# Optimization experiments

Measured on AMD Instinct MI355X. Metric: run time of the kernel, lower is better.

The kernel has to match this reference:

```python
import jax, jax.numpy as jnp
import numpy as np

B, H, S, DK, DV = 2, 16, 2048, 64, 64

def setup_inputs() -> dict:
    key = jax.random.key(0)
    kq, kk, kv, km = jax.random.split(key, 4)
    q = jax.random.normal(kq, (B, H, S, DK), dtype=jnp.float32)
    k = jax.random.normal(kk, (B, H, S, DK), dtype=jnp.float32)
    v = jax.random.normal(kv, (B, H, S, DV), dtype=jnp.float32)
    mask = jax.random.randint(km, (B, H, S, S), 0, 2).astype(jnp.bool_)
    return {"q": q, "k": k, "v": v, "mask": mask}

def reference(q, k, v, mask):
    d_k = q.shape[-1]
    # scores: [B, H, Sq, Sk]
    scores = jnp.einsum('bhqd,bhkd->bhqk', q, k) / np.sqrt(d_k).astype(jnp.float32)
    scores = jnp.where(mask, jnp.float32(-1e9), scores)
    attn = jax.nn.softmax(scores, axis=-1)
    return jnp.einsum('bhqk,bhkd->bhqd', attn, v)
```

## Files before the change

kernel.cpp:

```cpp
#include <hip/hip_runtime.h>


#define LOG2E 1.4426950408889634f
#define QSCALE (0.125f * LOG2E)

typedef __attribute__((ext_vector_type(8))) short short8;
typedef __attribute__((ext_vector_type(4))) short short4v;
typedef __attribute__((ext_vector_type(4))) float f32x4;

constexpr int S = 2048, D = 64;

__device__ __forceinline__ short bf16rne(float x) {
  union { float f; unsigned u; } cv; cv.f = x;
  unsigned u = cv.u;
  u += 0x7fffu + ((u >> 16) & 1u);
  return (short)(u >> 16);
}

__device__ __forceinline__ void glds16(const void* g, void* l) {
  __builtin_amdgcn_global_load_lds(
      (const __attribute__((address_space(1))) void*)g,
      (__attribute__((address_space(3))) void*)l, 16, 0, 0);
}

__global__ void detect_mask_fmt(const unsigned* __restrict__ m, int* __restrict__ flag) {
  unsigned v = m[threadIdx.x];
  unsigned long long big = __ballot(v > 1u && v != 0x3F800000u);
  unsigned long long isf = __ballot(v == 0x3F800000u);
  if (threadIdx.x == 0) *flag = (big != 0ull && isf == 0ull) ? 1 : 0;
}

__global__ void prep_k(const float* __restrict__ kp, short* __restrict__ kb) {
  size_t i = ((size_t)blockIdx.x * 256 + threadIdx.x) * 8;
  float4 a = *(const float4*)(kp + i);
  float4 b = *(const float4*)(kp + i + 4);
  short8 s;
  s[0] = bf16rne(a.x); s[1] = bf16rne(a.y); s[2] = bf16rne(a.z); s[3] = bf16rne(a.w);
  s[4] = bf16rne(b.x); s[5] = bf16rne(b.y); s[6] = bf16rne(b.z); s[7] = bf16rne(b.w);
  *(short8*)&kb[i] = s;
}

__global__ void prep_vt(const float* __restrict__ vp, short* __restrict__ vt) {
  __shared__ float tile[64][65];
  const int tid = threadIdx.x;
  const int bh = blockIdx.x >> 5, k0 = (blockIdx.x & 31) * 64;
  const float* src = vp + ((size_t)(bh * S + k0)) * D;
#pragma unroll
  for (int i = 0; i < 4; ++i) {
    int row = i * 16 + (tid >> 4);
    int col = (tid & 15) * 4;
    float4 x = *(const float4*)(src + row * D + col);
    tile[row][col] = x.x; tile[row][col + 1] = x.y;
    tile[row][col + 2] = x.z; tile[row][col + 3] = x.w;
  }
  __syncthreads();
#pragma unroll
  for (int i = 0; i < 4; ++i) {
    int dim = i * 16 + (tid >> 4);
    int kb4 = (tid & 15) * 4;
    short4v s;
#pragma unroll
    for (int j = 0; j < 4; ++j) s[j] = bf16rne(tile[kb4 + j][dim]);
    *(short4v*)&vt[((size_t)(bh * D + dim)) * S + k0 + kb4] = s;
  }
}

__launch_bounds__(256, 4)
__global__ void attn_fwd(const float* __restrict__ qp, const short* __restrict__ kb,
                         const short* __restrict__ vt, const void* __restrict__ mp,
                         float* __restrict__ op, const int* __restrict__ fmtp) {
  const int fmt  = *fmtp;
  const int tid  = threadIdx.x;
  const int lane = tid & 63;
  const int w    = tid >> 6;
  const int c    = lane & 15;
  const int quad = lane >> 4;

  const int bh = blockIdx.x >> 5;
  const int q0 = (blockIdx.x & 31) * 64;

  __shared__ short ks[64 * 64];
  __shared__ short vs[64 * 64];
  __shared__ short pst[4][16 * 72];

  const float* qg = qp + ((size_t)(bh * S + q0 + w * 16 + c)) * D;
  short8 qB[2];
#pragma unroll
  for (int kk = 0; kk < 2; ++kk) {
    const float* p = qg + kk * 32 + quad * 8;
    float4 x = *(const float4*)(p);
    float4 y = *(const float4*)(p + 4);
    short8 f;
    f[0] = bf16rne(x.x * QSCALE); f[1] = bf16rne(x.y * QSCALE);
    f[2] = bf16rne(x.z * QSCALE); f[3] = bf16rne(x.w * QSCALE);
    f[4] = bf16rne(y.x * QSCALE); f[5] = bf16rne(y.y * QSCALE);
    f[6] = bf16rne(y.z * QSCALE); f[7] = bf16rne(y.w * QSCALE);
    qB[kk] = f;
  }

  f32x4 O[4];
#pragma unroll
  for (int t = 0; t < 4; ++t) O[t] = (f32x4){0.f, 0.f, 0.f, 0.f};
  float L = 0.f;

  const int rsub = lane >> 3;
  const int csw  = (lane & 7) ^ rsub;
  const short* kbase = kb + ((size_t)(bh * S)) * D;
  const short* vbase = vt + ((size_t)(bh * D)) * S;

  const int sw0 = ((quad     ) ^ (c & 7)) * 8;
  const int sw1 = ((quad | 4 ) ^ (c & 7)) * 8;

  const size_t mrow = ((size_t)(bh * S + q0 + w * 16 + c)) * S;

  for (int it = 0; it < 32; ++it) {
    const int k0 = it * 64;
    __syncthreads();

#pragma unroll
    for (int h = 0; h < 2; ++h) {
      const int rbase = (h * 4 + w) * 8;
      const int row = rbase + rsub;
      glds16(kbase + (size_t)(k0 + row) * 64 + csw * 8,
             (char*)ks + (h * 4 + w) * 1024);
      glds16(vbase + (size_t)row * S + k0 + csw * 8,
             (char*)vs + (h * 4 + w) * 1024);
    }

    unsigned mb[4];
    if (fmt == 1) {
      const unsigned char* mq = (const unsigned char*)mp + mrow + k0 + 4 * quad;
#pragma unroll
      for (int t = 0; t < 4; ++t) mb[t] = *(const unsigned*)(mq + 16 * t);
    } else {
      const unsigned* mq = (const unsigned*)mp + mrow + k0 + 4 * quad;
#pragma unroll
      for (int t = 0; t < 4; ++t) {
        uint4 v = *(const uint4*)(mq + 16 * t);
        mb[t] = (v.x ? 1u : 0u) | (v.y ? 0x100u : 0u) |
                (v.z ? 0x10000u : 0u) | (v.w ? 0x1000000u : 0u);
      }
    }
    __syncthreads();

    float part = 0.f;
#pragma unroll
    for (int t = 0; t < 4; ++t) {
      short8 ka0 = *(const short8*)&ks[(16 * t + c) * 64 + sw0];
      short8 ka1 = *(const short8*)&ks[(16 * t + c) * 64 + sw1];
      f32x4 z = (f32x4){0.f, 0.f, 0.f, 0.f};
      z = __builtin_amdgcn_mfma_f32_16x16x32_bf16(ka0, qB[0], z, 0, 0, 0);
      z = __builtin_amdgcn_mfma_f32_16x16x32_bf16(ka1, qB[1], z, 0, 0, 0);
      short4v s4;
#pragma unroll
      for (int r = 0; r < 4; ++r) {
        float e = ((mb[t] >> (8 * r)) & 0xffu) ? 0.f : exp2f(z[r]);
        part += e;
        s4[r] = bf16rne(e);
      }
      *(short4v*)&pst[w][c * 72 + 16 * t + 4 * quad] = s4;
    }

    part += __shfl_xor(part, 16);
    part += __shfl_xor(part, 32);
    L += part;

    short8 pa0 = *(const short8*)&pst[w][c * 72 + quad * 8];
    short8 pa1 = *(const short8*)&pst[w][c * 72 + 32 + quad * 8];
#pragma unroll
    for (int t = 0; t < 4; ++t) {
      short8 vb0 = *(const short8*)&vs[(16 * t + c) * 64 + sw0];
      short8 vb1 = *(const short8*)&vs[(16 * t + c) * 64 + sw1];
      O[t] = __builtin_amdgcn_mfma_f32_16x16x32_bf16(pa0, vb0, O[t], 0, 0, 0);
      O[t] = __builtin_amdgcn_mfma_f32_16x16x32_bf16(pa1, vb1, O[t], 0, 0, 0);
    }
  }

#pragma unroll
  for (int r = 0; r < 4; ++r) {
    float Lr = __shfl(L, (lane & 48) | (quad * 4 + r));
    float inv = 1.f / Lr;
    const size_t ob = ((size_t)(bh * S + q0 + w * 16 + quad * 4 + r)) * D;
#pragma unroll
    for (int t = 0; t < 4; ++t) op[ob + 16 * t + c] = O[t][r] * inv;
  }
}

extern "C" void kernel_launch(void* const* d_in, const int* in_sizes, int n_in,
                              void* d_out, int out_size, void* d_ws, size_t ws_size,
                              hipStream_t stream) {
  const float* q = (const float*)d_in[0];
  const float* k = (const float*)d_in[1];
  const float* v = (const float*)d_in[2];
  const void*  m = d_in[3];

  short* kb  = (short*)d_ws;
  short* vtb = (short*)((char*)d_ws + (8u << 20));
  int* flag  = (int*)((char*)d_ws + (16u << 20));

  detect_mask_fmt<<<1, 64, 0, stream>>>((const unsigned*)m, flag);
  prep_k<<<2048, 256, 0, stream>>>(k, kb);
  prep_vt<<<1024, 256, 0, stream>>>(v, vtb);
  attn_fwd<<<1024, 256, 0, stream>>>(q, kb, vtb, m, (float*)d_out, flag);
}
```

Before: 754.7 us.

## Process 128 query rows per block and merge prep kernels into one launch

Each attention block now handles two 64-row query halves, so every K/V tile loaded into LDS feeds twice as many MFMAs. This halves the global-to-LDS K/V traffic per query and halves the grid to 512 blocks, with launch bounds lowered to 2 waves per SIMD for the extra registers. The three preprocessing kernels (mask format detection, K conversion, V transpose) are merged into one launch to cut launch overhead. The risks are lower occupancy, fewer blocks than CUs allow for latency hiding, and higher register pressure. The mask read, which dominates traffic, is unchanged.

Result: no change. 757.8 us (+0.4%).

```diff
diff --git a/kernel.cpp b/kernel.cpp
--- a/kernel.cpp
+++ b/kernel.cpp
@@ -23,49 +23,52 @@
       (__attribute__((address_space(3))) void*)l, 16, 0, 0);
 }
 
-__global__ void detect_mask_fmt(const unsigned* __restrict__ m, int* __restrict__ flag) {
-  unsigned v = m[threadIdx.x];
-  unsigned long long big = __ballot(v > 1u && v != 0x3F800000u);
-  unsigned long long isf = __ballot(v == 0x3F800000u);
-  if (threadIdx.x == 0) *flag = (big != 0ull && isf == 0ull) ? 1 : 0;
-}
-
-__global__ void prep_k(const float* __restrict__ kp, short* __restrict__ kb) {
-  size_t i = ((size_t)blockIdx.x * 256 + threadIdx.x) * 8;
-  float4 a = *(const float4*)(kp + i);
-  float4 b = *(const float4*)(kp + i + 4);
-  short8 s;
-  s[0] = bf16rne(a.x); s[1] = bf16rne(a.y); s[2] = bf16rne(a.z); s[3] = bf16rne(a.w);
-  s[4] = bf16rne(b.x); s[5] = bf16rne(b.y); s[6] = bf16rne(b.z); s[7] = bf16rne(b.w);
-  *(short8*)&kb[i] = s;
-}
-
-__global__ void prep_vt(const float* __restrict__ vp, short* __restrict__ vt) {
-  __shared__ float tile[64][65];
+__global__ void prep(const float* __restrict__ kp, const float* __restrict__ vp,
+                     short* __restrict__ kb, short* __restrict__ vt,
+                     const unsigned* __restrict__ m, int* __restrict__ flag) {
+  const int b = blockIdx.x;
   const int tid = threadIdx.x;
-  const int bh = blockIdx.x >> 5, k0 = (blockIdx.x & 31) * 64;
-  const float* src = vp + ((size_t)(bh * S + k0)) * D;
-#pragma unroll
-  for (int i = 0; i < 4; ++i) {
-    int row = i * 16 + (tid >> 4);
-    int col = (tid & 15) * 4;
-    float4 x = *(const float4*)(src + row * D + col);
-    tile[row][col] = x.x; tile[row][col + 1] = x.y;
-    tile[row][col + 2] = x.z; tile[row][col + 3] = x.w;
-  }
-  __syncthreads();
-#pragma unroll
-  for (int i = 0; i < 4; ++i) {
-    int dim = i * 16 + (tid >> 4);
-    int kb4 = (tid & 15) * 4;
-    short4v s;
-#pragma unroll
-    for (int j = 0; j < 4; ++j) s[j] = bf16rne(tile[kb4 + j][dim]);
-    *(short4v*)&vt[((size_t)(bh * D + dim)) * S + k0 + kb4] = s;
-  }
-}
-
-__launch_bounds__(256, 4)
+  if (b == 0 && tid < 64) {
+    unsigned v = m[tid];
+    unsigned long long big = __ballot(v > 1u && v != 0x3F800000u);
+    unsigned long long isf = __ballot(v == 0x3F800000u);
+    if (tid == 0) *flag = (big != 0ull && isf == 0ull) ? 1 : 0;
+  }
+  if (b < 2048) {
+    size_t i = ((size_t)b * 256 + tid) * 8;
+    float4 a = *(const float4*)(kp + i);
+    float4 c = *(const float4*)(kp + i + 4);
+    short8 s;
+    s[0] = bf16rne(a.x); s[1] = bf16rne(a.y); s[2] = bf16rne(a.z); s[3] = bf16rne(a.w);
+    s[4] = bf16rne(c.x); s[5] = bf16rne(c.y); s[6] = bf16rne(c.z); s[7] = bf16rne(c.w);
+    *(short8*)&kb[i] = s;
+  } else {
+    __shared__ float tile[64][65];
+    const int bb = b - 2048;
+    const int bh = bb >> 5, k0 = (bb & 31) * 64;
+    const float* src = vp + ((size_t)(bh * S + k0)) * D;
+#pragma unroll
+    for (int i = 0; i < 4; ++i) {
+      int row = i * 16 + (tid >> 4);
+      int col = (tid & 15) * 4;
+      float4 x = *(const float4*)(src + row * D + col);
+      tile[row][col] = x.x; tile[row][col + 1] = x.y;
+      tile[row][col + 2] = x.z; tile[row][col + 3] = x.w;
+    }
+    __syncthreads();
+#pragma unroll
+    for (int i = 0; i < 4; ++i) {
+      int dim = i * 16 + (tid >> 4);
+      int kb4 = (tid & 15) * 4;
+      short4v s;
+#pragma unroll
+      for (int j = 0; j < 4; ++j) s[j] = bf16rne(tile[kb4 + j][dim]);
+      *(short4v*)&vt[((size_t)(bh * D + dim)) * S + k0 + kb4] = s;
+    }
+  }
+}
+
+__launch_bounds__(256, 2)
 __global__ void attn_fwd(const float* __restrict__ qp, const short* __restrict__ kb,
                          const short* __restrict__ vt, const void* __restrict__ mp,
                          float* __restrict__ op, const int* __restrict__ fmtp) {
@@ -76,114 +79,142 @@
   const int c    = lane & 15;
   const int quad = lane >> 4;
 
-  const int bh = blockIdx.x >> 5;
-  const int q0 = (blockIdx.x & 31) * 64;
+  const int bh = blockIdx.x >> 4;
+  const int q0 = (blockIdx.x & 15) << 7;
 
   __shared__ short ks[64 * 64];
   __shared__ short vs[64 * 64];
-  __shared__ short pst[4][16 * 72];
-
-  const float* qg = qp + ((size_t)(bh * S + q0 + w * 16 + c)) * D;
-  short8 qB[2];
-#pragma unroll
-  for (int kk = 0; kk < 2; ++kk) {
-    const float* p = qg + kk * 32 + quad * 8;
-    float4 x = *(const float4*)(p);
-    float4 y = *(const float4*)(p + 4);
-    short8 f;
-    f[0] = bf16rne(x.x * QSCALE); f[1] = bf16rne(x.y * QSCALE);
-    f[2] = bf16rne(x.z * QSCALE); f[3] = bf16rne(x.w * QSCALE);
-    f[4] = bf16rne(y.x * QSCALE); f[5] = bf16rne(y.y * QSCALE);
-    f[6] = bf16rne(y.z * QSCALE); f[7] = bf16rne(y.w * QSCALE);
-    qB[kk] = f;
-  }
-
-  f32x4 O[4];
-#pragma unroll
-  for (int t = 0; t < 4; ++t) O[t] = (f32x4){0.f, 0.f, 0.f, 0.f};
-  float L = 0.f;
+  __shared__ short pst[4][32 * 72];
+
+  short8 qB[2][2];
+#pragma unroll
+  for (int h = 0; h < 2; ++h) {
+    const float* qg = qp + ((size_t)(bh * S + q0 + h * 64 + w * 16 + c)) * D;
+#pragma unroll
+    for (int kk = 0; kk < 2; ++kk) {
+      const float* p = qg + kk * 32 + quad * 8;
+      float4 x = *(const float4*)(p);
+      float4 y = *(const float4*)(p + 4);
+      short8 f;
+      f[0] = bf16rne(x.x * QSCALE); f[1] = bf16rne(x.y * QSCALE);
+      f[2] = bf16rne(x.z * QSCALE); f[3] = bf16rne(x.w * QSCALE);
+      f[4] = bf16rne(y.x * QSCALE); f[5] = bf16rne(y.y * QSCALE);
+      f[6] = bf16rne(y.z * QSCALE); f[7] = bf16rne(y.w * QSCALE);
+      qB[h][kk] = f;
+    }
+  }
+
+  f32x4 O[2][4];
+#pragma unroll
+  for (int h = 0; h < 2; ++h)
+#pragma unroll
+    for (int t = 0; t < 4; ++t) O[h][t] = (f32x4){0.f, 0.f, 0.f, 0.f};
+  float L[2] = {0.f, 0.f};
 
   const int rsub = lane >> 3;
   const int csw  = (lane & 7) ^ rsub;
   const short* kbase = kb + ((size_t)(bh * S)) * D;
   const short* vbase = vt + ((size_t)(bh * D)) * S;
 
-  const int sw0 = ((quad     ) ^ (c & 7)) * 8;
-  const int sw1 = ((quad | 4 ) ^ (c & 7)) * 8;
-
-  const size_t mrow = ((size_t)(bh * S + q0 + w * 16 + c)) * S;
+  const int sw0 = ((quad    ) ^ (c & 7)) * 8;
+  const int sw1 = ((quad | 4) ^ (c & 7)) * 8;
+
+  size_t mrow[2];
+#pragma unroll
+  for (int h = 0; h < 2; ++h)
+    mrow[h] = ((size_t)(bh * S + q0 + h * 64 + w * 16 + c)) * S;
 
   for (int it = 0; it < 32; ++it) {
     const int k0 = it * 64;
     __syncthreads();
 
 #pragma unroll
-    for (int h = 0; h < 2; ++h) {
-      const int rbase = (h * 4 + w) * 8;
-      const int row = rbase + rsub;
+    for (int h2 = 0; h2 < 2; ++h2) {
+      const int row = (h2 * 4 + w) * 8 + rsub;
       glds16(kbase + (size_t)(k0 + row) * 64 + csw * 8,
-             (char*)ks + (h * 4 + w) * 1024);
+             (char*)ks + (h2 * 4 + w) * 1024);
       glds16(vbase + (size_t)row * S + k0 + csw * 8,
-             (char*)vs + (h * 4 + w) * 1024);
-    }
-
-    unsigned mb[4];
+             (char*)vs + (h2 * 4 + w) * 1024);
+    }
+
+    unsigned mb[2][4];
     if (fmt == 1) {
-      const unsigned char* mq = (const unsigned char*)mp + mrow + k0 + 4 * quad;
-#pragma unroll
-      for (int t = 0; t < 4; ++t) mb[t] = *(const unsigned*)(mq + 16 * t);
+#pragma unroll
+      for (int h = 0; h < 2; ++h) {
+        const unsigned char* mq = (const unsigned char*)mp + mrow[h] + k0 + 4 * quad;
+#pragma unroll
+        for (int t = 0; t < 4; ++t) mb[h][t] = *(const unsigned*)(mq + 16 * t);
+      }
     } else {
-      const unsigned* mq = (const unsigned*)mp + mrow + k0 + 4 * quad;
-#pragma unroll
-      for (int t = 0; t < 4; ++t) {
-        uint4 v = *(const uint4*)(mq + 16 * t);
-        mb[t] = (v.x ? 1u : 0u) | (v.y ? 0x100u : 0u) |
-                (v.z ? 0x10000u : 0u) | (v.w ? 0x1000000u : 0u);
+#pragma unroll
+      for (int h = 0; h < 2; ++h) {
+        const unsigned* mq = (const unsigned*)mp + mrow[h] + k0 + 4 * quad;
+#pragma unroll
+        for (int t = 0; t < 4; ++t) {
+          uint4 v = *(const uint4*)(mq + 16 * t);
+          mb[h][t] = (v.x ? 1u : 0u) | (v.y ? 0x100u : 0u) |
+                     (v.z ? 0x10000u : 0u) | (v.w ? 0x1000000u : 0u);
+        }
       }
     }
     __syncthreads();
 
-    float part = 0.f;
+    float part[2] = {0.f, 0.f};
 #pragma unroll
     for (int t = 0; t < 4; ++t) {
       short8 ka0 = *(const short8*)&ks[(16 * t + c) * 64 + sw0];
       short8 ka1 = *(const short8*)&ks[(16 * t + c) * 64 + sw1];
-      f32x4 z = (f32x4){0.f, 0.f, 0.f, 0.f};
-      z = __builtin_amdgcn_mfma_f32_16x16x32_bf16(ka0, qB[0], z, 0, 0, 0);
-      z = __builtin_amdgcn_mfma_f32_16x16x32_bf16(ka1, qB[1], z, 0, 0, 0);
-      short4v s4;
-#pragma unroll
-      for (int r = 0; r < 4; ++r) {
-        float e = ((mb[t] >> (8 * r)) & 0xffu) ? 0.f : exp2f(z[r]);
-        part += e;
-        s4[r] = bf16rne(e);
-      }
-      *(short4v*)&pst[w][c * 72 + 16 * t + 4 * quad] = s4;
-    }
-
-    part += __shfl_xor(part, 16);
-    part += __shfl_xor(part, 32);
-    L += part;
-
-    short8 pa0 = *(const short8*)&pst[w][c * 72 + quad * 8];
-    short8 pa1 = *(const short8*)&pst[w][c * 72 + 32 + quad * 8];
+#pragma unroll
+      for (int h = 0; h < 2; ++h) {
+        f32x4 z = (f32x4){0.f, 0.f, 0.f, 0.f};
+        z = __builtin_amdgcn_mfma_f32_16x16x32_bf16(ka0, qB[h][0], z, 0, 0, 0);
+        z = __builtin_amdgcn_mfma_f32_16x16x32_bf16(ka1, qB[h][1], z, 0, 0, 0);
+        short4v s4;
+#pragma unroll
+        for (int r = 0; r < 4; ++r) {
+          float e = ((mb[h][t] >> (8 * r)) & 0xffu) ? 0.f : exp2f(z[r]);
+          part[h] += e;
+          s4[r] = bf16rne(e);
+        }
+        *(short4v*)&pst[w][(h * 16 + c) * 72 + 16 * t + 4 * quad] = s4;
+      }
+    }
+
+#pragma unroll
+    for (int h = 0; h < 2; ++h) {
+      part[h] += __shfl_xor(part[h], 16);
+      part[h] += __shfl_xor(part[h], 32);
+      L[h] += part[h];
+    }
+
+    short8 pa[2][2];
+#pragma unroll
+    for (int h = 0; h < 2; ++h) {
+      pa[h][0] = *(const short8*)&pst[w][(h * 16 + c) * 72 + quad * 8];
+      pa[h][1] = *(const short8*)&pst[w][(h * 16 + c) * 72 + 32 + quad * 8];
+    }
 #pragma unroll
     for (int t = 0; t < 4; ++t) {
       short8 vb0 = *(const short8*)&vs[(16 * t + c) * 64 + sw0];
       short8 vb1 = *(const short8*)&vs[(16 * t + c) * 64 + sw1];
-      O[t] = __builtin_amdgcn_mfma_f32_16x16x32_bf16(pa0, vb0, O[t], 0, 0, 0);
-      O[t] = __builtin_amdgcn_mfma_f32_16x16x32_bf16(pa1, vb1, O[t], 0, 0, 0);
-    }
-  }
-
-#pragma unroll
-  for (int r = 0; r < 4; ++r) {
-    float Lr = __shfl(L, (lane & 48) | (quad * 4 + r));
-    float inv = 1.f / Lr;
-    const size_t ob = ((size_t)(bh * S + q0 + w * 16 + quad * 4 + r)) * D;
-#pragma unroll
-    for (int t = 0; t < 4; ++t) op[ob + 16 * t + c] = O[t][r] * inv;
-  }
+#pragma unroll
+      for (int h = 0; h < 2; ++h) {
+        O[h][t] = __builtin_amdgcn_mfma_f32_16x16x32_bf16(pa[h][0], vb0, O[h][t], 0, 0, 0);
+        O[h][t] = __builtin_amdgcn_mfma_f32_16x16x32_bf16(pa[h][1], vb1, O[h][t], 0, 0, 0);
+      }
+    }
+  }
+
+#pragma unroll
+  for (int h = 0; h < 2; ++h)
+#pragma unroll
+    for (int r = 0; r < 4; ++r) {
+      float Lr = __shfl(L[h], (lane & 48) | (quad * 4 + r));
+      float inv = 1.f / Lr;
+      const size_t ob = ((size_t)(bh * S + q0 + h * 64 + w * 16 + quad * 4 + r)) * D;
+#pragma unroll
+      for (int t = 0; t < 4; ++t) op[ob + 16 * t + c] = O[h][t][r] * inv;
+    }
 }
 
 extern "C" void kernel_launch(void* const* d_in, const int* in_sizes, int n_in,
@@ -194,12 +225,10 @@
   const float* v = (const float*)d_in[2];
   const void*  m = d_in[3];
 
-  short* kb  = (short*)d_ws;
-  short* vtb = (short*)((char*)d_ws + (8u << 20));
-  int* flag  = (int*)((char*)d_ws + (16u << 20));
-
-  detect_mask_fmt<<<1, 64, 0, stream>>>((const unsigned*)m, flag);
-  prep_k<<<2048, 256, 0, stream>>>(k, kb);
-  prep_vt<<<1024, 256, 0, stream>>>(v, vtb);
-  attn_fwd<<<1024, 256, 0, stream>>>(q, kb, vtb, m, (float*)d_out, flag);
-}
+  short* kbuf = (short*)d_ws;
+  short* vtb  = (short*)((char*)d_ws + (8u << 20));
+  int* flag   = (int*)((char*)d_ws + (16u << 20));
+
+  prep<<<3072, 256, 0, stream>>>(k, v, kbuf, vtb, (const unsigned*)m, flag);
+  attn_fwd<<<512, 256, 0, stream>>>(q, kbuf, vtb, m, (float*)d_out, flag);
+}
```

## Double-buffer K/V tiles and prefetch mask, merge prep kernels into one launch

Applied to the files above, without the earlier changes.

The attention loop now double-buffers K and V in shared memory and loads the next tile and next mask chunk into registers while computing the current one. This removes one barrier per iteration and hides global load latency behind the MFMA and exp work. Mask loads use nontemporal hints. The three preprocessing kernels are merged into one launch to cut launch overhead. In exchange, shared memory and register use go up, and launch bounds are relaxed from 4 to 3 blocks per SM, which lowers occupancy.

New measurement: 778.1 us. 1.03x slower.

```diff
diff --git a/kernel.cpp b/kernel.cpp
--- a/kernel.cpp
+++ b/kernel.cpp
@@ -7,6 +7,7 @@
 typedef __attribute__((ext_vector_type(8))) short short8;
 typedef __attribute__((ext_vector_type(4))) short short4v;
 typedef __attribute__((ext_vector_type(4))) float f32x4;
+typedef unsigned __attribute__((ext_vector_type(4))) uintv4;
 
 constexpr int S = 2048, D = 64;
 
@@ -23,49 +24,52 @@
       (__attribute__((address_space(3))) void*)l, 16, 0, 0);
 }
 
-__global__ void detect_mask_fmt(const unsigned* __restrict__ m, int* __restrict__ flag) {
-  unsigned v = m[threadIdx.x];
-  unsigned long long big = __ballot(v > 1u && v != 0x3F800000u);
-  unsigned long long isf = __ballot(v == 0x3F800000u);
-  if (threadIdx.x == 0) *flag = (big != 0ull && isf == 0ull) ? 1 : 0;
-}
-
-__global__ void prep_k(const float* __restrict__ kp, short* __restrict__ kb) {
-  size_t i = ((size_t)blockIdx.x * 256 + threadIdx.x) * 8;
-  float4 a = *(const float4*)(kp + i);
-  float4 b = *(const float4*)(kp + i + 4);
-  short8 s;
-  s[0] = bf16rne(a.x); s[1] = bf16rne(a.y); s[2] = bf16rne(a.z); s[3] = bf16rne(a.w);
-  s[4] = bf16rne(b.x); s[5] = bf16rne(b.y); s[6] = bf16rne(b.z); s[7] = bf16rne(b.w);
-  *(short8*)&kb[i] = s;
-}
-
-__global__ void prep_vt(const float* __restrict__ vp, short* __restrict__ vt) {
-  __shared__ float tile[64][65];
+__global__ void prep(const float* __restrict__ kp, const float* __restrict__ vp,
+                     short* __restrict__ kb, short* __restrict__ vt,
+                     const unsigned* __restrict__ m, int* __restrict__ flag) {
+  const int b = blockIdx.x;
   const int tid = threadIdx.x;
-  const int bh = blockIdx.x >> 5, k0 = (blockIdx.x & 31) * 64;
-  const float* src = vp + ((size_t)(bh * S + k0)) * D;
-#pragma unroll
-  for (int i = 0; i < 4; ++i) {
-    int row = i * 16 + (tid >> 4);
-    int col = (tid & 15) * 4;
-    float4 x = *(const float4*)(src + row * D + col);
-    tile[row][col] = x.x; tile[row][col + 1] = x.y;
-    tile[row][col + 2] = x.z; tile[row][col + 3] = x.w;
-  }
-  __syncthreads();
-#pragma unroll
-  for (int i = 0; i < 4; ++i) {
-    int dim = i * 16 + (tid >> 4);
-    int kb4 = (tid & 15) * 4;
-    short4v s;
-#pragma unroll
-    for (int j = 0; j < 4; ++j) s[j] = bf16rne(tile[kb4 + j][dim]);
-    *(short4v*)&vt[((size_t)(bh * D + dim)) * S + k0 + kb4] = s;
-  }
-}
-
-__launch_bounds__(256, 4)
+  if (b == 0 && tid < 64) {
+    unsigned v = m[tid];
+    unsigned long long big = __ballot(v > 1u && v != 0x3F800000u);
+    unsigned long long isf = __ballot(v == 0x3F800000u);
+    if (tid == 0) *flag = (big != 0ull && isf == 0ull) ? 1 : 0;
+  }
+  if (b < 2048) {
+    size_t i = ((size_t)b * 256 + tid) * 8;
+    float4 a = *(const float4*)(kp + i);
+    float4 c = *(const float4*)(kp + i + 4);
+    short8 s;
+    s[0] = bf16rne(a.x); s[1] = bf16rne(a.y); s[2] = bf16rne(a.z); s[3] = bf16rne(a.w);
+    s[4] = bf16rne(c.x); s[5] = bf16rne(c.y); s[6] = bf16rne(c.z); s[7] = bf16rne(c.w);
+    *(short8*)&kb[i] = s;
+  } else {
+    __shared__ float tile[64][65];
+    const int bb = b - 2048;
+    const int bh = bb >> 5, k0 = (bb & 31) * 64;
+    const float* src = vp + ((size_t)(bh * S + k0)) * D;
+#pragma unroll
+    for (int i = 0; i < 4; ++i) {
+      int row = i * 16 + (tid >> 4);
+      int col = (tid & 15) * 4;
+      float4 x = *(const float4*)(src + row * D + col);
+      tile[row][col] = x.x; tile[row][col + 1] = x.y;
+      tile[row][col + 2] = x.z; tile[row][col + 3] = x.w;
+    }
+    __syncthreads();
+#pragma unroll
+    for (int i = 0; i < 4; ++i) {
+      int dim = i * 16 + (tid >> 4);
+      int kb4 = (tid & 15) * 4;
+      short4v s;
+#pragma unroll
+      for (int j = 0; j < 4; ++j) s[j] = bf16rne(tile[kb4 + j][dim]);
+      *(short4v*)&vt[((size_t)(bh * D + dim)) * S + k0 + kb4] = s;
+    }
+  }
+}
+
+__launch_bounds__(256, 3)
 __global__ void attn_fwd(const float* __restrict__ qp, const short* __restrict__ kb,
                          const short* __restrict__ vt, const void* __restrict__ mp,
                          float* __restrict__ op, const int* __restrict__ fmtp) {
@@ -79,8 +83,8 @@
   const int bh = blockIdx.x >> 5;
   const int q0 = (blockIdx.x & 31) * 64;
 
-  __shared__ short ks[64 * 64];
-  __shared__ short vs[64 * 64];
+  __shared__ short ks[2][64 * 64];
+  __shared__ short vs[2][64 * 64];
   __shared__ short pst[4][16 * 72];
 
   const float* qg = qp + ((size_t)(bh * S + q0 + w * 16 + c)) * D;
@@ -108,46 +112,77 @@
   const short* kbase = kb + ((size_t)(bh * S)) * D;
   const short* vbase = vt + ((size_t)(bh * D)) * S;
 
-  const int sw0 = ((quad     ) ^ (c & 7)) * 8;
-  const int sw1 = ((quad | 4 ) ^ (c & 7)) * 8;
+  const int sw0 = ((quad    ) ^ (c & 7)) * 8;
+  const int sw1 = ((quad | 4) ^ (c & 7)) * 8;
 
   const size_t mrow = ((size_t)(bh * S + q0 + w * 16 + c)) * S;
 
+  uintv4  mr4[4];
+  unsigned mr1[4];
+
+#pragma unroll
+  for (int h2 = 0; h2 < 2; ++h2) {
+    const int row = (h2 * 4 + w) * 8 + rsub;
+    glds16(kbase + (size_t)row * 64 + csw * 8, (char*)&ks[0][0] + (h2 * 4 + w) * 1024);
+    glds16(vbase + (size_t)row * S + csw * 8,  (char*)&vs[0][0] + (h2 * 4 + w) * 1024);
+  }
+  if (fmt == 1) {
+    const unsigned char* mq = (const unsigned char*)mp + mrow + 4 * quad;
+#pragma unroll
+    for (int t = 0; t < 4; ++t)
+      mr1[t] = __builtin_nontemporal_load((const unsigned*)(mq + 16 * t));
+  } else {
+    const uintv4* mq = (const uintv4*)((const unsigned*)mp + mrow + 4 * quad);
+#pragma unroll
+    for (int t = 0; t < 4; ++t)
+      mr4[t] = __builtin_nontemporal_load(mq + 4 * t);
+  }
+
   for (int it = 0; it < 32; ++it) {
-    const int k0 = it * 64;
+    const int cur = it & 1;
     __syncthreads();
-
-#pragma unroll
-    for (int h = 0; h < 2; ++h) {
-      const int rbase = (h * 4 + w) * 8;
-      const int row = rbase + rsub;
-      glds16(kbase + (size_t)(k0 + row) * 64 + csw * 8,
-             (char*)ks + (h * 4 + w) * 1024);
-      glds16(vbase + (size_t)row * S + k0 + csw * 8,
-             (char*)vs + (h * 4 + w) * 1024);
-    }
 
     unsigned mb[4];
     if (fmt == 1) {
-      const unsigned char* mq = (const unsigned char*)mp + mrow + k0 + 4 * quad;
-#pragma unroll
-      for (int t = 0; t < 4; ++t) mb[t] = *(const unsigned*)(mq + 16 * t);
+#pragma unroll
+      for (int t = 0; t < 4; ++t) mb[t] = mr1[t];
     } else {
-      const unsigned* mq = (const unsigned*)mp + mrow + k0 + 4 * quad;
 #pragma unroll
       for (int t = 0; t < 4; ++t) {
-        uint4 v = *(const uint4*)(mq + 16 * t);
-        mb[t] = (v.x ? 1u : 0u) | (v.y ? 0x100u : 0u) |
-                (v.z ? 0x10000u : 0u) | (v.w ? 0x1000000u : 0u);
-      }
-    }
-    __syncthreads();
+        uintv4 v = mr4[t];
+        mb[t] = (v[0] ? 1u : 0u) | (v[1] ? 0x100u : 0u) |
+                (v[2] ? 0x10000u : 0u) | (v[3] ? 0x1000000u : 0u);
+      }
+    }
+
+    if (it + 1 < 32) {
+      const int k1 = (it + 1) * 64;
+#pragma unroll
+      for (int h2 = 0; h2 < 2; ++h2) {
+        const int row = (h2 * 4 + w) * 8 + rsub;
+        glds16(kbase + (size_t)(k1 + row) * 64 + csw * 8,
+               (char*)&ks[cur ^ 1][0] + (h2 * 4 + w) * 1024);
+        glds16(vbase + (size_t)row * S + k1 + csw * 8,
+               (char*)&vs[cur ^ 1][0] + (h2 * 4 + w) * 1024);
+      }
+      if (fmt == 1) {
+        const unsigned char* mq = (const unsigned char*)mp + mrow + k1 + 4 * quad;
+#pragma unroll
+        for (int t = 0; t < 4; ++t)
+          mr1[t] = __builtin_nontemporal_load((const unsigned*)(mq + 16 * t));
+      } else {
+        const uintv4* mq = (const uintv4*)((const unsigned*)mp + mrow + k1 + 4 * quad);
+#pragma unroll
+        for (int t = 0; t < 4; ++t)
+          mr4[t] = __builtin_nontemporal_load(mq + 4 * t);
+      }
+    }
 
     float part = 0.f;
 #pragma unroll
     for (int t = 0; t < 4; ++t) {
-      short8 ka0 = *(const short8*)&ks[(16 * t + c) * 64 + sw0];
-      short8 ka1 = *(const short8*)&ks[(16 * t + c) * 64 + sw1];
+      short8 ka0 = *(const short8*)&ks[cur][(16 * t + c) * 64 + sw0];
+      short8 ka1 = *(const short8*)&ks[cur][(16 * t + c) * 64 + sw1];
       f32x4 z = (f32x4){0.f, 0.f, 0.f, 0.f};
       z = __builtin_amdgcn_mfma_f32_16x16x32_bf16(ka0, qB[0], z, 0, 0, 0);
       z = __builtin_amdgcn_mfma_f32_16x16x32_bf16(ka1, qB[1], z, 0, 0, 0);
@@ -169,8 +204,8 @@
     short8 pa1 = *(const short8*)&pst[w][c * 72 + 32 + quad * 8];
 #pragma unroll
     for (int t = 0; t < 4; ++t) {
-      short8 vb0 = *(const short8*)&vs[(16 * t + c) * 64 + sw0];
-      short8 vb1 = *(const short8*)&vs[(16 * t + c) * 64 + sw1];
+      short8 vb0 = *(const short8*)&vs[cur][(16 * t + c) * 64 + sw0];
+      short8 vb1 = *(const short8*)&vs[cur][(16 * t + c) * 64 + sw1];
       O[t] = __builtin_amdgcn_mfma_f32_16x16x32_bf16(pa0, vb0, O[t], 0, 0, 0);
       O[t] = __builtin_amdgcn_mfma_f32_16x16x32_bf16(pa1, vb1, O[t], 0, 0, 0);
     }
@@ -194,12 +229,10 @@
   const float* v = (const float*)d_in[2];
   const void*  m = d_in[3];
 
-  short* kb  = (short*)d_ws;
-  short* vtb = (short*)((char*)d_ws + (8u << 20));
-  int* flag  = (int*)((char*)d_ws + (16u << 20));
-
-  detect_mask_fmt<<<1, 64, 0, stream>>>((const unsigned*)m, flag);
-  prep_k<<<2048, 256, 0, stream>>>(k, kb);
-  prep_vt<<<1024, 256, 0, stream>>>(v, vtb);
-  attn_fwd<<<1024, 256, 0, stream>>>(q, kb, vtb, m, (float*)d_out, flag);
-}
+  short* kbuf = (short*)d_ws;
+  short* vtb  = (short*)((char*)d_ws + (8u << 20));
+  int* flag   = (int*)((char*)d_ws + (16u << 20));
+
+  prep<<<3072, 256, 0, stream>>>(k, v, kbuf, vtb, (const unsigned*)m, flag);
+  attn_fwd<<<1024, 256, 0, stream>>>(q, kbuf, vtb, m, (float*)d_out, flag);
+}
```
